# Kernel optimization log

Measured on AMD Instinct MI355X. Metric: run time of the kernel, lower is better.

Reference implementation:

```python
import math
import jax, jax.numpy as jnp
import numpy as np

T, B, IN, H, D, ETA, R = 128, 32, 512, 8, 64, 4, 4
DE = ETA * D  # expanded key dim = eta * head_dim
EPS = 1e-05


def setup_inputs() -> dict:
    key = jax.random.key(0)
    ks = jax.random.split(key, 8)
    s = 0.05
    return {
        "inputs": jax.random.normal(ks[0], (T, B, IN), jnp.float32),
        "terminations": jnp.zeros((T, B), jnp.float32),
        "tilde_k_prev": jax.random.normal(ks[1], (B, R, H, DE), jnp.float32) * s,
        "tilde_v_prev": jax.random.normal(ks[2], (B, R, H, D), jnp.float32) * s,
        "s_prev": jax.random.normal(ks[3], (B, H, DE), jnp.float32) * s,
        "tick": jnp.zeros((B, 1), jnp.float32),
        "W_kqv": jax.random.normal(ks[4], (H * D * 5, IN), jnp.float32) * s,
        "b_kqv": jnp.zeros((H * D * 5,), jnp.float32),
        "W_p": jax.random.normal(ks[5], (H * ETA * 3, IN), jnp.float32) * s,
        "b_p": jnp.zeros((H * ETA * 3,), jnp.float32),
        "W_o": jax.random.normal(ks[6], (IN, H * D), jnp.float32) * s,
        "b_o": jnp.zeros((IN,), jnp.float32),
    }


def _forward(inputs, terminations, tilde_k_prev, tilde_v_prev, s_prev, tick,
             W_kqv, b_kqv, W_p, b_p, W_o, b_o):
    # projections
    kqv = (inputs @ W_kqv.T + b_kqv).reshape(T, B, H, 5, D)
    keys, queries, values, beta, gammas = (kqv[..., i, :] for i in range(5))
    p = (inputs @ W_p.T + b_p).reshape(T, B, H, 3, ETA)
    p1, p2, p3 = (p[..., i, :] for i in range(3))
    relu, sig = jax.nn.relu, jax.nn.sigmoid
    # kernel feature maps: outer product then flatten (d outer, n inner)
    keys = jnp.einsum('tbhd,tbhn->tbhdn', relu(keys), relu(p1)).reshape(T, B, H, DE)
    queries = jnp.einsum('tbhd,tbhn->tbhdn', relu(queries), relu(p2)).reshape(T, B, H, DE)
    gammas = jnp.einsum('tbhd,tbhn->tbhdn', sig(gammas), sig(p3)).reshape(T, B, H, DE)
    beta = sig(beta)  # (T,B,H,D)
    # oscillatory basis
    ticks = tick[None] + jnp.arange(1, T + 1, dtype=jnp.float32).reshape(T, 1, 1)  # (T,B,1)
    omegas = jnp.linspace(-math.pi, math.pi, R)
    occil = jnp.cos(ticks * omegas[None, None, :])  # (T,B,R)
    values = values * beta
    values_r = values[:, :, None] * occil[:, :, :, None, None]   # (T,B,R,H,D)
    keys_g = keys * gammas                                        # (T,B,H,DE)
    keys_r = keys_g[:, :, None] * occil[:, :, :, None, None]     # (T,B,R,H,DE)
    # discounts (with termination resets)
    nt = (1.0 - terminations)[:, :, None, None]
    dg = (1.0 - gammas) * nt  # (T,B,H,DE)
    db = (1.0 - beta) * nt    # (T,B,H,D)
    # recurrence y[t] = discount[t]*y[t-1] + x[t] via lax.scan over T
    def step(carry, xs):
        k_st, v_st, s_st = carry
        kx, vx, sx, dgt, dbt = xs
        k_new = dgt[:, None] * k_st + kx   # (B,R,H,DE)
        v_new = dbt[:, None] * v_st + vx   # (B,R,H,D)
        s_new = dgt * s_st + sx            # (B,H,DE)
        return (k_new, v_new, s_new), (k_new, v_new, s_new)
    (kf, vf, sf), (K, V, S) = jax.lax.scan(
        step, (tilde_k_prev, tilde_v_prev, s_prev), (keys_r, values_r, keys_g, dg, db))
    # attention readout
    kdq = jnp.einsum('tbrhd,tbhd->tbrh', K, queries)
    kv = jnp.einsum('tbrhd,tbrh->tbhd', V, kdq)
    norm = jnp.einsum('tbhd,tbhd->tbh', S, queries)
    attn = kv / (2 * R * norm[..., None] + EPS)  # (T,B,H,D)
    out = attn.reshape(T, B, H * D) @ W_o.T + b_o  # dropout p=0 (eval)
    return out, kf, vf, sf, tick + T


def reference(inputs, terminations, tilde_k_prev, tilde_v_prev, s_prev, tick,
              W_kqv, b_kqv, W_p, b_p, W_o, b_o):
    return _forward(inputs, terminations, tilde_k_prev, tilde_v_prev, s_prev, tick,
                    W_kqv, b_kqv, W_p, b_p, W_o, b_o)
```

## Files before the change

### kernel.cpp

```cpp
#include <hip/hip_runtime.h>
#include <math.h>
#include <stdint.h>

constexpr int T_ = 128, B_ = 32, IN_ = 512, H_ = 8, D_ = 64, ETA_ = 4, R_ = 4;
constexpr int DE_ = ETA_ * D_;
constexpr float EPS_ = 1e-5f;
constexpr int M_   = T_ * B_;
constexpr int NCH  = 8;
constexpr int CH   = T_ / NCH;
constexpr int BH_  = B_ * H_;

constexpr int NW = 2688;
constexpr int SPLITCOL = 1664;

typedef __attribute__((ext_vector_type(8))) short bf16x8;
typedef __attribute__((ext_vector_type(4))) float f32x4;

__device__ __forceinline__ float bf2f(unsigned short u) {
    return __builtin_bit_cast(float, ((unsigned)u) << 16);
}
__device__ __forceinline__ unsigned short f2bf(float f) {
    unsigned u = __builtin_bit_cast(unsigned, f);
    u = (u + 0x7fffu + ((u >> 16) & 1u)) >> 16;
    return (unsigned short)u;
}
__device__ __forceinline__ float fsigm(float x) {
    return __fdividef(1.f, 1.f + __expf(-x));
}

__global__ __launch_bounds__(256) void cast_splitA(
    const float* __restrict__ src, unsigned short* __restrict__ dst, int n4)
{
    int i = blockIdx.x * 256 + threadIdx.x;
    if (i >= n4) return;
    const int r = i >> 7;
    const int c = (i & 127) << 2;
    float4 x = *(const float4*)(src + (size_t)r * 512 + c);
    ushort4 hi = make_ushort4(f2bf(x.x), f2bf(x.y), f2bf(x.z), f2bf(x.w));
    ushort4 lo = make_ushort4(f2bf(x.x - bf2f(hi.x)), f2bf(x.y - bf2f(hi.y)),
                              f2bf(x.z - bf2f(hi.z)), f2bf(x.w - bf2f(hi.w)));
    unsigned short* dr = dst + (size_t)r * 1024 + c;
    *(ushort4*)dr = hi;
    *(ushort4*)(dr + 512) = lo;
}

__global__ __launch_bounds__(256) void build_w2_bias(
    const float* __restrict__ Wkqv, const float* __restrict__ Wp,
    const float* __restrict__ bkqv, const float* __restrict__ bp,
    unsigned short* __restrict__ W2, float* __restrict__ bias_perm)
{
    int i = blockIdx.x * 256 + threadIdx.x;
    if (i >= NW * 128) return;
    const int rr = i >> 7;
    const int c = (i & 127) << 2;

    bool zero = false;
    const float* srow = nullptr;
    float bv = 0.f;
    if (rr < 512) {
        const int h = rr >> 6, dd = rr & 63, s = h * 320 + dd;
        srow = Wkqv + (size_t)s * 512; bv = bkqv[s];
    } else if (rr < 1024) {
        const int q = rr - 512, h = q >> 6, dd = q & 63, s = h * 320 + 64 + dd;
        srow = Wkqv + (size_t)s * 512; bv = bkqv[s];
    } else if (rr < 1536) {
        const int q = rr - 1024, h = q >> 6, dd = q & 63, s = h * 320 + 256 + dd;
        srow = Wkqv + (size_t)s * 512; bv = bkqv[s];
    } else if (rr < 1632) {
        const int q = rr - 1536;
        srow = Wp + (size_t)q * 512; bv = bp[q];
    } else if (rr < 1664) {
        zero = true;
    } else if (rr < 2176) {
        const int q = rr - 1664, h = q >> 6, dd = q & 63, s = h * 320 + 128 + dd;
        srow = Wkqv + (size_t)s * 512; bv = bkqv[s];
    } else {
        const int q = rr - 2176, h = q >> 6, dd = q & 63, s = h * 320 + 192 + dd;
        srow = Wkqv + (size_t)s * 512; bv = bkqv[s];
    }

    float4 x = zero ? make_float4(0.f, 0.f, 0.f, 0.f) : *(const float4*)(srow + c);
    ushort4 hi = make_ushort4(f2bf(x.x), f2bf(x.y), f2bf(x.z), f2bf(x.w));
    ushort4 lo = make_ushort4(f2bf(x.x - bf2f(hi.x)), f2bf(x.y - bf2f(hi.y)),
                              f2bf(x.z - bf2f(hi.z)), f2bf(x.w - bf2f(hi.w)));
    unsigned short* dr = W2 + (size_t)rr * 1536 + c;
    *(ushort4*)dr = hi;
    *(ushort4*)(dr + 512) = lo;
    *(ushort4*)(dr + 1024) = hi;
    if (c == 0) bias_perm[rr] = zero ? 0.f : bv;
}

__global__ __launch_bounds__(256) void cast_f32_bf16(
    const float* __restrict__ src, unsigned short* __restrict__ dst, int n8)
{
    int i = blockIdx.x * 256 + threadIdx.x;
    if (i >= n8) return;
    const float4* s = (const float4*)src;
    float4 a = s[2 * i], b = s[2 * i + 1];
    *(ushort4*)(dst + 8 * i)     = make_ushort4(f2bf(a.x), f2bf(a.y), f2bf(a.z), f2bf(a.w));
    *(ushort4*)(dst + 8 * i + 4) = make_ushort4(f2bf(b.x), f2bf(b.y), f2bf(b.z), f2bf(b.w));
}

__device__ __forceinline__ void gl_lds16(const unsigned short* g, unsigned short* l) {
    __builtin_amdgcn_global_load_lds((const __attribute__((address_space(1))) void*)g,
                                     (__attribute__((address_space(3))) void*)l, 16, 0, 0);
}

template <int BM, int BN>
__global__ __launch_bounds__(256) void gemm_bf16(
    const unsigned short* __restrict__ A,
    const unsigned short* __restrict__ W,
    const float* __restrict__ bias,
    float* __restrict__ C,
    int N, int sA, int sW, int kBig, int kSmall, int splitcol)
{
    constexpr int WM = BM / 2, WN = BN / 2;
    constexpr int AM = WM / 16, AN = WN / 16;
    constexpr int NLA = BM / 64;
    constexpr int NLB = BN / 64;
    constexpr int NLD = NLA + NLB;

    int bx, by;
    {
        const int nwg = gridDim.x * gridDim.y;
        int lin = blockIdx.y * gridDim.x + blockIdx.x;
        lin = (lin & 7) * (nwg >> 3) + (lin >> 3);
        const int G = (gridDim.x % 7 == 0) ? 7 : gridDim.x;
        const int grpsz = gridDim.y * G;
        const int cg = lin / grpsz, rem = lin % grpsz;
        by = rem / G;
        bx = cg * G + rem % G;
    }
    const int bm = by * BM;
    const int bn = bx * BN;
    const int tid = threadIdx.x;
    const int lane = tid & 63;
    const int wid = tid >> 6;
    const int wr = wid >> 1;
    const int wc = wid & 1;

    __shared__ __align__(16) unsigned short As[3][BM * 32];
    __shared__ __align__(16) unsigned short Bs[3][BN * 32];

    const unsigned short* aRow = A + (size_t)(bm + (tid & (BM - 1))) * sA
                                   + (tid / BM) * 8;
    const unsigned short* bRow = W + (size_t)(bn + (tid & (BN - 1))) * sW
                                   + (tid / BN) * 8;

    const int fA = (((lane >> 4) * BM) + wr * WM + (lane & 15)) * 8;
    const int fB = (((lane >> 4) * BN) + wc * WN + (lane & 15)) * 8;

    f32x4 acc[AM][AN] = {};
    const int K = (bn < splitcol) ? kBig : kSmall;
    const int NKT = K >> 5;

    auto stage = [&](int buf, int k0) {
        const int koA = (k0 >= 512) ? k0 - 512 : k0;
#pragma unroll
        for (int i = 0; i < NLA; ++i)
            gl_lds16(aRow + koA + i * (256 / BM) * 8,
                     &As[buf][(i * 256 + wid * 64) * 8]);
#pragma unroll
        for (int i = 0; i < NLB; ++i)
            gl_lds16(bRow + k0 + i * (256 / BN) * 8,
                     &Bs[buf][(i * 256 + wid * 64) * 8]);
    };

    stage(0, 0);
    if (NKT > 1) stage(1, 32);

    for (int kt = 0; kt < NKT; ++kt) {
        const int cur = kt % 3;
        if (kt + 2 < NKT) {
            stage((kt + 2) % 3, (kt + 2) << 5);
            if constexpr (NLD == 4)      asm volatile("s_waitcnt vmcnt(8)\ns_barrier" ::: "memory");
            else if constexpr (NLD == 3) asm volatile("s_waitcnt vmcnt(6)\ns_barrier" ::: "memory");
            else                         asm volatile("s_waitcnt vmcnt(4)\ns_barrier" ::: "memory");
        } else if (kt + 2 == NKT) {
            if constexpr (NLD == 4)      asm volatile("s_waitcnt vmcnt(4)\ns_barrier" ::: "memory");
            else if constexpr (NLD == 3) asm volatile("s_waitcnt vmcnt(3)\ns_barrier" ::: "memory");
            else                         asm volatile("s_waitcnt vmcnt(2)\ns_barrier" ::: "memory");
        } else {
            asm volatile("s_waitcnt vmcnt(0)\ns_barrier" ::: "memory");
        }
        __builtin_amdgcn_sched_barrier(0);

        bf16x8 af[AM], bfr[AN];
#pragma unroll
        for (int m = 0; m < AM; ++m) af[m] = *(const bf16x8*)&As[cur][fA + m * 128];
#pragma unroll
        for (int n = 0; n < AN; ++n) bfr[n] = *(const bf16x8*)&Bs[cur][fB + n * 128];
#pragma unroll
        for (int m = 0; m < AM; ++m)
#pragma unroll
            for (int n = 0; n < AN; ++n)
                acc[m][n] = __builtin_amdgcn_mfma_f32_16x16x32_bf16(af[m], bfr[n], acc[m][n], 0, 0, 0);

        asm volatile("s_waitcnt lgkmcnt(0)\ns_barrier" ::: "memory");
    }

#pragma unroll
    for (int n = 0; n < AN; ++n) {
        const int col = bn + wc * WN + n * 16 + (lane & 15);
        const float bv = bias[col];
#pragma unroll
        for (int m = 0; m < AM; ++m) {
            const int row0 = bm + wr * WM + m * 16 + ((lane >> 4) << 2);
#pragma unroll
            for (int j = 0; j < 4; ++j)
                C[(size_t)(row0 + j) * N + col] = acc[m][n][j] + bv;
        }
    }
}

template <int CTRL, int RM>
__device__ __forceinline__ float dpp_radd(float x) {
    int t = __builtin_amdgcn_update_dpp(0, __builtin_bit_cast(int, x), CTRL, RM, 0xf, true);
    return x + __builtin_bit_cast(float, t);
}
__device__ __forceinline__ float wave_allsum(float x) {
    x = dpp_radd<0x111, 0xf>(x);
    x = dpp_radd<0x112, 0xf>(x);
    x = dpp_radd<0x114, 0xf>(x);
    x = dpp_radd<0x118, 0xf>(x);
    x = dpp_radd<0x142, 0xa>(x);
    x = dpp_radd<0x143, 0xc>(x);
    return __builtin_bit_cast(float, __builtin_amdgcn_readlane(__builtin_bit_cast(int, x), 63));
}

__device__ __forceinline__ void osc2(float tt, float& oc03, float& oc12) {
    oc03 = cosf(3.14159265358979323846f * tt);
    oc12 = cosf(1.04719755119659774615f * tt);
}


__global__ __launch_bounds__(64) void scanA(
    const float* __restrict__ kqv, const float* __restrict__ term,
    const float* __restrict__ tick,
    float* __restrict__ Dg, float* __restrict__ Db,
    float* __restrict__ Kloc, float* __restrict__ Vloc, float* __restrict__ Sloc)
{
    const int bh = blockIdx.x & (BH_ - 1);
    const int c  = blockIdx.x >> 8;
    const int b = bh >> 3, h = bh & 7;
    const int d = threadIdx.x;

    float K0[4] = {}, K1[4] = {}, K2[4] = {}, K3[4] = {}, S[4] = {};
    float V0 = 0.f, V1 = 0.f, V2 = 0.f, V3 = 0.f;
    float Dgv[4] = {1.f, 1.f, 1.f, 1.f};
    float Dbv = 1.f;
    const float tk = tick[b];

    for (int t = c * CH; t < (c + 1) * CH; ++t) {
        const float* row = kqv + ((size_t)t * B_ + b) * NW;
        const float c0 = row[h * 64 + d];
        const float c2 = row[1664 + h * 64 + d];
        const float c3 = row[2176 + h * 64 + d];
        const float c4 = row[1024 + h * 64 + d];
        const float* pr = row + 1536 + h * 12;
        const float4 p1 = *(const float4*)pr;
        const float4 p3 = *(const float4*)(pr + 8);
        const float nt = 1.f - term[(size_t)t * B_ + b];

        float oc03, oc12; osc2(tk + (float)(t + 1), oc03, oc12);
        const float sgam = fsigm(c4);
        const float rk = fmaxf(c0, 0.f);
        const float sbet = fsigm(c3);
        const float vb = c2 * sbet;
        const float dbv = (1.f - sbet) * nt;
        const float p1a[4] = {p1.x, p1.y, p1.z, p1.w};
        const float p3a[4] = {p3.x, p3.y, p3.z, p3.w};
#pragma unroll
        for (int n = 0; n < 4; ++n) {
            const float g  = sgam * fsigm(p3a[n]);
            const float kg = rk * fmaxf(p1a[n], 0.f) * g;
            const float dg = (1.f - g) * nt;
            S[n]  = fmaf(dg, S[n],  kg);
            K0[n] = fmaf(dg, K0[n], kg * oc03);
            K1[n] = fmaf(dg, K1[n], kg * oc12);
            K2[n] = fmaf(dg, K2[n], kg * oc12);
            K3[n] = fmaf(dg, K3[n], kg * oc03);
            Dgv[n] *= dg;
        }
        V0 = fmaf(dbv, V0, vb * oc03);
        V1 = fmaf(dbv, V1, vb * oc12);
        V2 = fmaf(dbv, V2, vb * oc12);
        V3 = fmaf(dbv, V3, vb * oc03);
        Dbv *= dbv;
    }

    const size_t cb = (size_t)c * BH_ + bh;
    *(float4*)&Dg[cb * DE_ + 4 * d] = make_float4(Dgv[0], Dgv[1], Dgv[2], Dgv[3]);
    Db[cb * D_ + d] = Dbv;
    *(float4*)&Kloc[(cb * 4 + 0) * DE_ + 4 * d] = make_float4(K0[0], K0[1], K0[2], K0[3]);
    *(float4*)&Kloc[(cb * 4 + 1) * DE_ + 4 * d] = make_float4(K1[0], K1[1], K1[2], K1[3]);
    *(float4*)&Kloc[(cb * 4 + 2) * DE_ + 4 * d] = make_float4(K2[0], K2[1], K2[2], K2[3]);
    *(float4*)&Kloc[(cb * 4 + 3) * DE_ + 4 * d] = make_float4(K3[0], K3[1], K3[2], K3[3]);
    Vloc[(cb * 4 + 0) * D_ + d] = V0;
    Vloc[(cb * 4 + 1) * D_ + d] = V1;
    Vloc[(cb * 4 + 2) * D_ + d] = V2;
    Vloc[(cb * 4 + 3) * D_ + d] = V3;
    *(float4*)&Sloc[cb * DE_ + 4 * d] = make_float4(S[0], S[1], S[2], S[3]);
}

__global__ __launch_bounds__(256) void scanB(
    const float* __restrict__ k_prev, const float* __restrict__ v_prev,
    const float* __restrict__ s_prev,
    float* __restrict__ Dg, float* __restrict__ Db,
    float* __restrict__ Kloc, float* __restrict__ Vloc, float* __restrict__ Sloc)
{
    const int bh = blockIdx.x;
    const int b = bh >> 3, h = bh & 7;
    const int de = threadIdx.x;

    float Kin[4], Sin, Vin[4];
#pragma unroll
    for (int r = 0; r < 4; ++r)
        Kin[r] = k_prev[((size_t)(b * 4 + r) * 8 + h) * DE_ + de];
    Sin = s_prev[((size_t)b * 8 + h) * DE_ + de];
    if (de < D_) {
#pragma unroll
        for (int r = 0; r < 4; ++r)
            Vin[r] = v_prev[((size_t)(b * 4 + r) * 8 + h) * D_ + de];
    }

    for (int c = 0; c < NCH; ++c) {
        const size_t cb = (size_t)c * BH_ + bh;
        const float dg = Dg[cb * DE_ + de];
#pragma unroll
        for (int r = 0; r < 4; ++r) {
            const size_t ix = (cb * 4 + r) * DE_ + de;
            const float kl = Kloc[ix];
            Kloc[ix] = Kin[r];
            Kin[r] = fmaf(dg, Kin[r], kl);
        }
        {
            const size_t ix = cb * DE_ + de;
            const float sl = Sloc[ix];
            Sloc[ix] = Sin;
            Sin = fmaf(dg, Sin, sl);
        }
        if (de < D_) {
            const float db = Db[cb * D_ + de];
#pragma unroll
            for (int r = 0; r < 4; ++r) {
                const size_t ix = (cb * 4 + r) * D_ + de;
                const float vl = Vloc[ix];
                Vloc[ix] = Vin[r];
                Vin[r] = fmaf(db, Vin[r], vl);
            }
        }
    }
}

__global__ __launch_bounds__(64) void scanC(
    const float* __restrict__ kqv, const float* __restrict__ term,
    const float* __restrict__ tick,
    const float* __restrict__ Kloc, const float* __restrict__ Vloc,
    const float* __restrict__ Sloc,
    unsigned short* __restrict__ attn,
    float* __restrict__ kf, float* __restrict__ vf, float* __restrict__ sf,
    float* __restrict__ tick_out)
{
    const int bh = blockIdx.x & (BH_ - 1);
    const int c  = blockIdx.x >> 8;
    const int b = bh >> 3, h = bh & 7;
    const int d = threadIdx.x;
    const size_t cb = (size_t)c * BH_ + bh;

    float K0[4], K1[4], K2[4], K3[4], S[4];
    float V0, V1, V2, V3;
    {
        float4 k4;
        k4 = *(const float4*)&Kloc[(cb * 4 + 0) * DE_ + 4 * d];
        K0[0] = k4.x; K0[1] = k4.y; K0[2] = k4.z; K0[3] = k4.w;
        k4 = *(const float4*)&Kloc[(cb * 4 + 1) * DE_ + 4 * d];
        K1[0] = k4.x; K1[1] = k4.y; K1[2] = k4.z; K1[3] = k4.w;
        k4 = *(const float4*)&Kloc[(cb * 4 + 2) * DE_ + 4 * d];
        K2[0] = k4.x; K2[1] = k4.y; K2[2] = k4.z; K2[3] = k4.w;
        k4 = *(const float4*)&Kloc[(cb * 4 + 3) * DE_ + 4 * d];
        K3[0] = k4.x; K3[1] = k4.y; K3[2] = k4.z; K3[3] = k4.w;
        k4 = *(const float4*)&Sloc[cb * DE_ + 4 * d];
        S[0] = k4.x; S[1] = k4.y; S[2] = k4.z; S[3] = k4.w;
        V0 = Vloc[(cb * 4 + 0) * D_ + d];
        V1 = Vloc[(cb * 4 + 1) * D_ + d];
        V2 = Vloc[(cb * 4 + 2) * D_ + d];
        V3 = Vloc[(cb * 4 + 3) * D_ + d];
    }
    const float tk = tick[b];

    for (int t = c * CH; t < (c + 1) * CH; ++t) {
        const float* row = kqv + ((size_t)t * B_ + b) * NW;
        const float c0 = row[h * 64 + d];
        const float c1 = row[512 + h * 64 + d];
        const float c2 = row[1664 + h * 64 + d];
        const float c3 = row[2176 + h * 64 + d];
        const float c4 = row[1024 + h * 64 + d];
        const float* pr = row + 1536 + h * 12;
        const float4 p1 = *(const float4*)pr;
        const float4 p2 = *(const float4*)(pr + 4);
        const float4 p3 = *(const float4*)(pr + 8);
        const float nt = 1.f - term[(size_t)t * B_ + b];

        float oc03, oc12; osc2(tk + (float)(t + 1), oc03, oc12);
        const float sgam = fsigm(c4);
        const float rk = fmaxf(c0, 0.f);
        const float rq = fmaxf(c1, 0.f);
        const float sbet = fsigm(c3);
        const float vb = c2 * sbet;
        const float dbv = (1.f - sbet) * nt;
        const float p1a[4] = {p1.x, p1.y, p1.z, p1.w};
        const float p2a[4] = {p2.x, p2.y, p2.z, p2.w};
        const float p3a[4] = {p3.x, p3.y, p3.z, p3.w};

        float s0 = 0.f, s1 = 0.f, s2 = 0.f, s3 = 0.f, s4 = 0.f;
#pragma unroll
        for (int n = 0; n < 4; ++n) {
            const float g  = sgam * fsigm(p3a[n]);
            const float kg = rk * fmaxf(p1a[n], 0.f) * g;
            const float qe = rq * fmaxf(p2a[n], 0.f);
            const float dg = (1.f - g) * nt;
            S[n]  = fmaf(dg, S[n],  kg);
            K0[n] = fmaf(dg, K0[n], kg * oc03);
            K1[n] = fmaf(dg, K1[n], kg * oc12);
            K2[n] = fmaf(dg, K2[n], kg * oc12);
            K3[n] = fmaf(dg, K3[n], kg * oc03);
            s0 = fmaf(K0[n], qe, s0);
            s1 = fmaf(K1[n], qe, s1);
            s2 = fmaf(K2[n], qe, s2);
            s3 = fmaf(K3[n], qe, s3);
            s4 = fmaf(S[n],  qe, s4);
        }
        V0 = fmaf(dbv, V0, vb * oc03);
        V1 = fmaf(dbv, V1, vb * oc12);
        V2 = fmaf(dbv, V2, vb * oc12);
        V3 = fmaf(dbv, V3, vb * oc03);

        const float kdq0 = wave_allsum(s0);
        const float kdq1 = wave_allsum(s1);
        const float kdq2 = wave_allsum(s2);
        const float kdq3 = wave_allsum(s3);
        const float nrm  = wave_allsum(s4);

        const float kv = V0 * kdq0 + V1 * kdq1 + V2 * kdq2 + V3 * kdq3;
        attn[((size_t)t * B_ + b) * (H_ * D_) + h * D_ + d] =
            f2bf(__fdividef(kv, 2.f * (float)R_ * nrm + EPS_));
    }

    if (c == NCH - 1) {
        *(float4*)&kf[((size_t)(b * 4 + 0) * 8 + h) * DE_ + 4 * d] = make_float4(K0[0], K0[1], K0[2], K0[3]);
        *(float4*)&kf[((size_t)(b * 4 + 1) * 8 + h) * DE_ + 4 * d] = make_float4(K1[0], K1[1], K1[2], K1[3]);
        *(float4*)&kf[((size_t)(b * 4 + 2) * 8 + h) * DE_ + 4 * d] = make_float4(K2[0], K2[1], K2[2], K2[3]);
        *(float4*)&kf[((size_t)(b * 4 + 3) * 8 + h) * DE_ + 4 * d] = make_float4(K3[0], K3[1], K3[2], K3[3]);
        *(float4*)&sf[((size_t)b * 8 + h) * DE_ + 4 * d] = make_float4(S[0], S[1], S[2], S[3]);
        vf[((size_t)(b * 4 + 0) * 8 + h) * D_ + d] = V0;
        vf[((size_t)(b * 4 + 1) * 8 + h) * D_ + d] = V1;
        vf[((size_t)(b * 4 + 2) * 8 + h) * D_ + d] = V2;
        vf[((size_t)(b * 4 + 3) * 8 + h) * D_ + d] = V3;
        if (h == 0 && d == 0) tick_out[b] = tk + (float)T_;
    }
}

extern "C" void kernel_launch(void* const* d_in, const int* in_sizes, int n_in,
                              void* d_out, int out_size, void* d_ws, size_t ws_size,
                              hipStream_t stream)
{
    const float* inputs = (const float*)d_in[0];
    const float* term   = (const float*)d_in[1];
    const float* k_prev = (const float*)d_in[2];
    const float* v_prev = (const float*)d_in[3];
    const float* s_prev = (const float*)d_in[4];
    const float* tick   = (const float*)d_in[5];
    const float* W_kqv  = (const float*)d_in[6];
    const float* b_kqv  = (const float*)d_in[7];
    const float* W_p    = (const float*)d_in[8];
    const float* b_p    = (const float*)d_in[9];
    const float* W_o    = (const float*)d_in[10];
    const float* b_o    = (const float*)d_in[11];

    float* out = (float*)d_out;
    float* kf  = out + (size_t)T_ * B_ * IN_;
    float* vf  = kf  + (size_t)B_ * R_ * H_ * DE_;
    float* sf  = vf  + (size_t)B_ * R_ * H_ * D_;
    float* tick_out = sf + (size_t)B_ * H_ * DE_;

    float* kqv_s = (float*)d_ws;
    unsigned short* attn_bf = (unsigned short*)(kqv_s + (size_t)M_ * NW);
    unsigned short* Wo_bf   = attn_bf + (size_t)M_ * IN_;
    unsigned short* A2      = Wo_bf + (size_t)IN_ * (H_ * D_);
    unsigned short* W2      = A2 + (size_t)M_ * 1024;
    float* bias_perm        = (float*)(W2 + (size_t)NW * 1536);

    float* Dg   = (float*)A2;
    float* Db   = Dg   + (size_t)NCH * BH_ * DE_;
    float* Kloc = Db   + (size_t)NCH * BH_ * D_;
    float* Vloc = Kloc + (size_t)NCH * BH_ * 4 * DE_;
    float* Sloc = Vloc + (size_t)NCH * BH_ * 4 * D_;

    {
        int n4 = M_ * 128;
        cast_splitA<<<(n4 + 255) / 256, 256, 0, stream>>>(inputs, A2, n4);
        n4 = NW * 128;
        build_w2_bias<<<(n4 + 255) / 256, 256, 0, stream>>>(W_kqv, W_p, b_kqv, b_p,
                                                            W2, bias_perm);
        int n8 = (IN_ * (H_ * D_)) / 8;
        cast_f32_bf16<<<(n8 + 255) / 256, 256, 0, stream>>>(W_o, Wo_bf, n8);
    }

    {
        dim3 grid(NW / 128, M_ / 128);
        gemm_bf16<128, 128><<<grid, 256, 0, stream>>>(A2, W2, bias_perm, kqv_s,
                                                      NW, 1024, 1536, 1536, 512, SPLITCOL);
    }

    scanA<<<NCH * BH_, 64, 0, stream>>>(kqv_s, term, tick, Dg, Db, Kloc, Vloc, Sloc);
    scanB<<<BH_, 256, 0, stream>>>(k_prev, v_prev, s_prev, Dg, Db, Kloc, Vloc, Sloc);
    scanC<<<NCH * BH_, 64, 0, stream>>>(kqv_s, term, tick, Kloc, Vloc, Sloc,
                                        attn_bf, kf, vf, sf, tick_out);

    {
        dim3 grid(IN_ / 64, M_ / 64);
        gemm_bf16<64, 64><<<grid, 256, 0, stream>>>(attn_bf, Wo_bf, b_o, out,
                                                    IN_, 512, 512, 512, 512, 0);
    }
}
```

Baseline: 154.1 us.

## Fuse three-pass chunked scan into one kernel with LDS carry propagation

The three scan kernels (local chunk scan, carry propagation, rescan with readout) are merged into one 1024-thread block per (batch, head). Each of its 16 waves scans an 8-step chunk, and chunk summaries are exchanged through shared memory instead of global workspace. This removes two kernel launches and the global round-trips for Dg/Db/Kloc/Vloc/Sloc. In exchange only 256 blocks run, the carry propagation is serialized inside each block, and shared memory use is large (~90KB), which limits occupancy.

```diff
diff --git a/kernel.cpp b/kernel.cpp
--- a/kernel.cpp
+++ b/kernel.cpp
@@ -6,9 +6,9 @@
 constexpr int DE_ = ETA_ * D_;
 constexpr float EPS_ = 1e-5f;
 constexpr int M_   = T_ * B_;
-constexpr int NCH  = 8;
-constexpr int CH   = T_ / NCH;
 constexpr int BH_  = B_ * H_;
+constexpr int NC2  = 16;
+constexpr int CH2  = T_ / NC2;
 
 constexpr int NW = 2688;
 constexpr int SPLITCOL = 1664;
@@ -233,25 +233,53 @@
     oc12 = cosf(1.04719755119659774615f * tt);
 }
 
-
-__global__ __launch_bounds__(64) void scanA(
+__global__ __launch_bounds__(1024) void scan_fused(
     const float* __restrict__ kqv, const float* __restrict__ term,
     const float* __restrict__ tick,
-    float* __restrict__ Dg, float* __restrict__ Db,
-    float* __restrict__ Kloc, float* __restrict__ Vloc, float* __restrict__ Sloc)
+    const float* __restrict__ k_prev, const float* __restrict__ v_prev,
+    const float* __restrict__ s_prev,
+    unsigned short* __restrict__ attn,
+    float* __restrict__ kf, float* __restrict__ vf, float* __restrict__ sf,
+    float* __restrict__ tick_out)
 {
-    const int bh = blockIdx.x & (BH_ - 1);
-    const int c  = blockIdx.x >> 8;
+    const int bh = blockIdx.x;
     const int b = bh >> 3, h = bh & 7;
-    const int d = threadIdx.x;
+    const int tid = threadIdx.x;
+    const int w = tid >> 6;
+    const int d = tid & 63;
+
+    __shared__ float LK[NC2][4][DE_];
+    __shared__ float LS[NC2][DE_];
+    __shared__ float LV[NC2][4][D_];
+    __shared__ float LDg[NC2][DE_];
+    __shared__ float LDb[NC2][D_];
+
+    const float tk = tick[b];
 
     float K0[4] = {}, K1[4] = {}, K2[4] = {}, K3[4] = {}, S[4] = {};
     float V0 = 0.f, V1 = 0.f, V2 = 0.f, V3 = 0.f;
     float Dgv[4] = {1.f, 1.f, 1.f, 1.f};
     float Dbv = 1.f;
-    const float tk = tick[b];
-
-    for (int t = c * CH; t < (c + 1) * CH; ++t) {
+
+    if (w == 0) {
+        float4 k4;
+        k4 = *(const float4*)&k_prev[((size_t)(b * 4 + 0) * 8 + h) * DE_ + 4 * d];
+        K0[0] = k4.x; K0[1] = k4.y; K0[2] = k4.z; K0[3] = k4.w;
+        k4 = *(const float4*)&k_prev[((size_t)(b * 4 + 1) * 8 + h) * DE_ + 4 * d];
+        K1[0] = k4.x; K1[1] = k4.y; K1[2] = k4.z; K1[3] = k4.w;
+        k4 = *(const float4*)&k_prev[((size_t)(b * 4 + 2) * 8 + h) * DE_ + 4 * d];
+        K2[0] = k4.x; K2[1] = k4.y; K2[2] = k4.z; K2[3] = k4.w;
+        k4 = *(const float4*)&k_prev[((size_t)(b * 4 + 3) * 8 + h) * DE_ + 4 * d];
+        K3[0] = k4.x; K3[1] = k4.y; K3[2] = k4.z; K3[3] = k4.w;
+        k4 = *(const float4*)&s_prev[((size_t)b * 8 + h) * DE_ + 4 * d];
+        S[0] = k4.x; S[1] = k4.y; S[2] = k4.z; S[3] = k4.w;
+        V0 = v_prev[((size_t)(b * 4 + 0) * 8 + h) * D_ + d];
+        V1 = v_prev[((size_t)(b * 4 + 1) * 8 + h) * D_ + d];
+        V2 = v_prev[((size_t)(b * 4 + 2) * 8 + h) * D_ + d];
+        V3 = v_prev[((size_t)(b * 4 + 3) * 8 + h) * D_ + d];
+    }
+
+    for (int t = w * CH2; t < w * CH2 + CH2; ++t) {
         const float* row = kqv + ((size_t)t * B_ + b) * NW;
         const float c0 = row[h * 64 + d];
         const float c2 = row[1664 + h * 64 + d];
@@ -289,107 +317,83 @@
         Dbv *= dbv;
     }
 
-    const size_t cb = (size_t)c * BH_ + bh;
-    *(float4*)&Dg[cb * DE_ + 4 * d] = make_float4(Dgv[0], Dgv[1], Dgv[2], Dgv[3]);
-    Db[cb * D_ + d] = Dbv;
-    *(float4*)&Kloc[(cb * 4 + 0) * DE_ + 4 * d] = make_float4(K0[0], K0[1], K0[2], K0[3]);
-    *(float4*)&Kloc[(cb * 4 + 1) * DE_ + 4 * d] = make_float4(K1[0], K1[1], K1[2], K1[3]);
-    *(float4*)&Kloc[(cb * 4 + 2) * DE_ + 4 * d] = make_float4(K2[0], K2[1], K2[2], K2[3]);
-    *(float4*)&Kloc[(cb * 4 + 3) * DE_ + 4 * d] = make_float4(K3[0], K3[1], K3[2], K3[3]);
-    Vloc[(cb * 4 + 0) * D_ + d] = V0;
-    Vloc[(cb * 4 + 1) * D_ + d] = V1;
-    Vloc[(cb * 4 + 2) * D_ + d] = V2;
-    Vloc[(cb * 4 + 3) * D_ + d] = V3;
-    *(float4*)&Sloc[cb * DE_ + 4 * d] = make_float4(S[0], S[1], S[2], S[3]);
-}
-
-__global__ __launch_bounds__(256) void scanB(
-    const float* __restrict__ k_prev, const float* __restrict__ v_prev,
-    const float* __restrict__ s_prev,
-    float* __restrict__ Dg, float* __restrict__ Db,
-    float* __restrict__ Kloc, float* __restrict__ Vloc, float* __restrict__ Sloc)
-{
-    const int bh = blockIdx.x;
-    const int b = bh >> 3, h = bh & 7;
-    const int de = threadIdx.x;
-
-    float Kin[4], Sin, Vin[4];
-#pragma unroll
-    for (int r = 0; r < 4; ++r)
-        Kin[r] = k_prev[((size_t)(b * 4 + r) * 8 + h) * DE_ + de];
-    Sin = s_prev[((size_t)b * 8 + h) * DE_ + de];
-    if (de < D_) {
-#pragma unroll
-        for (int r = 0; r < 4; ++r)
-            Vin[r] = v_prev[((size_t)(b * 4 + r) * 8 + h) * D_ + de];
-    }
-
-    for (int c = 0; c < NCH; ++c) {
-        const size_t cb = (size_t)c * BH_ + bh;
-        const float dg = Dg[cb * DE_ + de];
-#pragma unroll
-        for (int r = 0; r < 4; ++r) {
-            const size_t ix = (cb * 4 + r) * DE_ + de;
-            const float kl = Kloc[ix];
-            Kloc[ix] = Kin[r];
-            Kin[r] = fmaf(dg, Kin[r], kl);
+    *(float4*)&LK[w][0][4 * d] = make_float4(K0[0], K0[1], K0[2], K0[3]);
+    *(float4*)&LK[w][1][4 * d] = make_float4(K1[0], K1[1], K1[2], K1[3]);
+    *(float4*)&LK[w][2][4 * d] = make_float4(K2[0], K2[1], K2[2], K2[3]);
+    *(float4*)&LK[w][3][4 * d] = make_float4(K3[0], K3[1], K3[2], K3[3]);
+    *(float4*)&LS[w][4 * d]    = make_float4(S[0], S[1], S[2], S[3]);
+    LV[w][0][d] = V0; LV[w][1][d] = V1; LV[w][2][d] = V2; LV[w][3][d] = V3;
+    *(float4*)&LDg[w][4 * d]   = make_float4(Dgv[0], Dgv[1], Dgv[2], Dgv[3]);
+    LDb[w][d] = Dbv;
+    __syncthreads();
+
+    if (tid < DE_) {
+        const int de = tid;
+        float c0 = LK[0][0][de], c1k = LK[0][1][de], c2k = LK[0][2][de],
+              c3k = LK[0][3][de], cs = LS[0][de];
+        for (int c = 1; c < NC2; ++c) {
+            const float dg = LDg[c][de];
+            float n0 = fmaf(dg, c0,  LK[c][0][de]); LK[c][0][de] = c0;  c0  = n0;
+            float n1 = fmaf(dg, c1k, LK[c][1][de]); LK[c][1][de] = c1k; c1k = n1;
+            float n2 = fmaf(dg, c2k, LK[c][2][de]); LK[c][2][de] = c2k; c2k = n2;
+            float n3 = fmaf(dg, c3k, LK[c][3][de]); LK[c][3][de] = c3k; c3k = n3;
+            float ns = fmaf(dg, cs,  LS[c][de]);    LS[c][de]    = cs;  cs  = ns;
         }
-        {
-            const size_t ix = cb * DE_ + de;
-            const float sl = Sloc[ix];
-            Sloc[ix] = Sin;
-            Sin = fmaf(dg, Sin, sl);
+        kf[((size_t)(b * 4 + 0) * 8 + h) * DE_ + de] = c0;
+        kf[((size_t)(b * 4 + 1) * 8 + h) * DE_ + de] = c1k;
+        kf[((size_t)(b * 4 + 2) * 8 + h) * DE_ + de] = c2k;
+        kf[((size_t)(b * 4 + 3) * 8 + h) * DE_ + de] = c3k;
+        sf[((size_t)b * 8 + h) * DE_ + de] = cs;
+    } else if (tid < DE_ + D_) {
+        const int dd = tid - DE_;
+        float v0 = LV[0][0][dd], v1 = LV[0][1][dd], v2 = LV[0][2][dd], v3 = LV[0][3][dd];
+        for (int c = 1; c < NC2; ++c) {
+            const float db = LDb[c][dd];
+            float n0 = fmaf(db, v0, LV[c][0][dd]); LV[c][0][dd] = v0; v0 = n0;
+            float n1 = fmaf(db, v1, LV[c][1][dd]); LV[c][1][dd] = v1; v1 = n1;
+            float n2 = fmaf(db, v2, LV[c][2][dd]); LV[c][2][dd] = v2; v2 = n2;
+            float n3 = fmaf(db, v3, LV[c][3][dd]); LV[c][3][dd] = v3; v3 = n3;
         }
-        if (de < D_) {
-            const float db = Db[cb * D_ + de];
-#pragma unroll
-            for (int r = 0; r < 4; ++r) {
-                const size_t ix = (cb * 4 + r) * D_ + de;
-                const float vl = Vloc[ix];
-                Vloc[ix] = Vin[r];
-                Vin[r] = fmaf(db, Vin[r], vl);
-            }
-        }
-    }
-}
-
-__global__ __launch_bounds__(64) void scanC(
-    const float* __restrict__ kqv, const float* __restrict__ term,
-    const float* __restrict__ tick,
-    const float* __restrict__ Kloc, const float* __restrict__ Vloc,
-    const float* __restrict__ Sloc,
-    unsigned short* __restrict__ attn,
-    float* __restrict__ kf, float* __restrict__ vf, float* __restrict__ sf,
-    float* __restrict__ tick_out)
-{
-    const int bh = blockIdx.x & (BH_ - 1);
-    const int c  = blockIdx.x >> 8;
-    const int b = bh >> 3, h = bh & 7;
-    const int d = threadIdx.x;
-    const size_t cb = (size_t)c * BH_ + bh;
-
-    float K0[4], K1[4], K2[4], K3[4], S[4];
-    float V0, V1, V2, V3;
-    {
+        vf[((size_t)(b * 4 + 0) * 8 + h) * D_ + dd] = v0;
+        vf[((size_t)(b * 4 + 1) * 8 + h) * D_ + dd] = v1;
+        vf[((size_t)(b * 4 + 2) * 8 + h) * D_ + dd] = v2;
+        vf[((size_t)(b * 4 + 3) * 8 + h) * D_ + dd] = v3;
+    }
+    if (h == 0 && tid == 0) tick_out[b] = tk + (float)T_;
+    __syncthreads();
+
+    if (w == 0) {
         float4 k4;
-        k4 = *(const float4*)&Kloc[(cb * 4 + 0) * DE_ + 4 * d];
+        k4 = *(const float4*)&k_prev[((size_t)(b * 4 + 0) * 8 + h) * DE_ + 4 * d];
         K0[0] = k4.x; K0[1] = k4.y; K0[2] = k4.z; K0[3] = k4.w;
-        k4 = *(const float4*)&Kloc[(cb * 4 + 1) * DE_ + 4 * d];
+        k4 = *(const float4*)&k_prev[((size_t)(b * 4 + 1) * 8 + h) * DE_ + 4 * d];
         K1[0] = k4.x; K1[1] = k4.y; K1[2] = k4.z; K1[3] = k4.w;
-        k4 = *(const float4*)&Kloc[(cb * 4 + 2) * DE_ + 4 * d];
+        k4 = *(const float4*)&k_prev[((size_t)(b * 4 + 2) * 8 + h) * DE_ + 4 * d];
         K2[0] = k4.x; K2[1] = k4.y; K2[2] = k4.z; K2[3] = k4.w;
-        k4 = *(const float4*)&Kloc[(cb * 4 + 3) * DE_ + 4 * d];
+        k4 = *(const float4*)&k_prev[((size_t)(b * 4 + 3) * 8 + h) * DE_ + 4 * d];
         K3[0] = k4.x; K3[1] = k4.y; K3[2] = k4.z; K3[3] = k4.w;
-        k4 = *(const float4*)&Sloc[cb * DE_ + 4 * d];
+        k4 = *(const float4*)&s_prev[((size_t)b * 8 + h) * DE_ + 4 * d];
         S[0] = k4.x; S[1] = k4.y; S[2] = k4.z; S[3] = k4.w;
-        V0 = Vloc[(cb * 4 + 0) * D_ + d];
-        V1 = Vloc[(cb * 4 + 1) * D_ + d];
-        V2 = Vloc[(cb * 4 + 2) * D_ + d];
-        V3 = Vloc[(cb * 4 + 3) * D_ + d];
-    }
-    const float tk = tick[b];
-
-    for (int t = c * CH; t < (c + 1) * CH; ++t) {
+        V0 = v_prev[((size_t)(b * 4 + 0) * 8 + h) * D_ + d];
+        V1 = v_prev[((size_t)(b * 4 + 1) * 8 + h) * D_ + d];
+        V2 = v_prev[((size_t)(b * 4 + 2) * 8 + h) * D_ + d];
+        V3 = v_prev[((size_t)(b * 4 + 3) * 8 + h) * D_ + d];
+    } else {
+        float4 k4;
+        k4 = *(const float4*)&LK[w][0][4 * d];
+        K0[0] = k4.x; K0[1] = k4.y; K0[2] = k4.z; K0[3] = k4.w;
+        k4 = *(const float4*)&LK[w][1][4 * d];
+        K1[0] = k4.x; K1[1] = k4.y; K1[2] = k4.z; K1[3] = k4.w;
+        k4 = *(const float4*)&LK[w][2][4 * d];
+        K2[0] = k4.x; K2[1] = k4.y; K2[2] = k4.z; K2[3] = k4.w;
+        k4 = *(const float4*)&LK[w][3][4 * d];
+        K3[0] = k4.x; K3[1] = k4.y; K3[2] = k4.z; K3[3] = k4.w;
+        k4 = *(const float4*)&LS[w][4 * d];
+        S[0] = k4.x; S[1] = k4.y; S[2] = k4.z; S[3] = k4.w;
+        V0 = LV[w][0][d]; V1 = LV[w][1][d]; V2 = LV[w][2][d]; V3 = LV[w][3][d];
+    }
+
+    for (int t = w * CH2; t < w * CH2 + CH2; ++t) {
         const float* row = kqv + ((size_t)t * B_ + b) * NW;
         const float c0 = row[h * 64 + d];
         const float c1 = row[512 + h * 64 + d];
@@ -446,19 +450,6 @@
         attn[((size_t)t * B_ + b) * (H_ * D_) + h * D_ + d] =
             f2bf(__fdividef(kv, 2.f * (float)R_ * nrm + EPS_));
     }
-
-    if (c == NCH - 1) {
-        *(float4*)&kf[((size_t)(b * 4 + 0) * 8 + h) * DE_ + 4 * d] = make_float4(K0[0], K0[1], K0[2], K0[3]);
-        *(float4*)&kf[((size_t)(b * 4 + 1) * 8 + h) * DE_ + 4 * d] = make_float4(K1[0], K1[1], K1[2], K1[3]);
-        *(float4*)&kf[((size_t)(b * 4 + 2) * 8 + h) * DE_ + 4 * d] = make_float4(K2[0], K2[1], K2[2], K2[3]);
-        *(float4*)&kf[((size_t)(b * 4 + 3) * 8 + h) * DE_ + 4 * d] = make_float4(K3[0], K3[1], K3[2], K3[3]);
-        *(float4*)&sf[((size_t)b * 8 + h) * DE_ + 4 * d] = make_float4(S[0], S[1], S[2], S[3]);
-        vf[((size_t)(b * 4 + 0) * 8 + h) * D_ + d] = V0;
-        vf[((size_t)(b * 4 + 1) * 8 + h) * D_ + d] = V1;
-        vf[((size_t)(b * 4 + 2) * 8 + h) * D_ + d] = V2;
-        vf[((size_t)(b * 4 + 3) * 8 + h) * D_ + d] = V3;
-        if (h == 0 && d == 0) tick_out[b] = tk + (float)T_;
-    }
 }
 
 extern "C" void kernel_launch(void* const* d_in, const int* in_sizes, int n_in,
@@ -491,12 +482,6 @@
     unsigned short* W2      = A2 + (size_t)M_ * 1024;
     float* bias_perm        = (float*)(W2 + (size_t)NW * 1536);
 
-    float* Dg   = (float*)A2;
-    float* Db   = Dg   + (size_t)NCH * BH_ * DE_;
-    float* Kloc = Db   + (size_t)NCH * BH_ * D_;
-    float* Vloc = Kloc + (size_t)NCH * BH_ * 4 * DE_;
-    float* Sloc = Vloc + (size_t)NCH * BH_ * 4 * D_;
-
     {
         int n4 = M_ * 128;
         cast_splitA<<<(n4 + 255) / 256, 256, 0, stream>>>(inputs, A2, n4);
@@ -513,10 +498,8 @@
                                                       NW, 1024, 1536, 1536, 512, SPLITCOL);
     }
 
-    scanA<<<NCH * BH_, 64, 0, stream>>>(kqv_s, term, tick, Dg, Db, Kloc, Vloc, Sloc);
-    scanB<<<BH_, 256, 0, stream>>>(k_prev, v_prev, s_prev, Dg, Db, Kloc, Vloc, Sloc);
-    scanC<<<NCH * BH_, 64, 0, stream>>>(kqv_s, term, tick, Kloc, Vloc, Sloc,
-                                        attn_bf, kf, vf, sf, tick_out);
+    scan_fused<<<BH_, 1024, 0, stream>>>(kqv_s, term, tick, k_prev, v_prev, s_prev,
+                                         attn_bf, kf, vf, sf, tick_out);
 
     {
         dim3 grid(IN_ / 64, M_ / 64);
```

Result: faster. 139.0 us (median of 3 runs) (-9.8%).
